# Optimization experiments

Measured on AMD Instinct MI355X. Metric: run time of the kernel, lower is better.

The kernel has to match this reference:

```python
import jax, jax.numpy as jnp
import numpy as np

# Module constants (match init_kwargs)
M = 2049                      # NpointsMesh (odd)
TAU = 2.821e-5                # Gaussian spreading width ~ 12*(pi/M)^2
XLIMS = (0.0, 10.0)
L = abs(XLIMS[1] - XLIMS[0])
KGRID = jnp.asarray(np.linspace(-(M // 2), M // 2, M), dtype=jnp.float32)        # (M,)
XGRID = jnp.asarray(2.0 * np.pi * np.linspace(XLIMS[0], XLIMS[1], M + 1)[:-1] / L,
                    dtype=jnp.float32)                                           # (M,)
FOUR_PI = 4.0 * np.pi


def setup_inputs() -> dict:
    key = jax.random.key(0)
    kx, = jax.random.split(key, 1)
    x = jax.random.uniform(kx, (16, 1024), dtype=jnp.float32) * 10.0  # points in [xLims[0], xLims[1])
    ones = jnp.ones((1,), dtype=jnp.float32)  # tf.initializers.ones for all 4 weights
    return {"x": x, "shift0": ones, "amp0": ones, "shift1": ones, "amp1": ones}


def reference(x, shift0, amp0, shift1, amp1):
    # Gaussian spreading: (B, N, M)
    diff = x[..., None] * (2.0 * np.pi / L) - XGRID
    g = jnp.exp(-jnp.square(diff) / (4.0 * TAU))
    # Sum over points -> gridded density (B, M), then FFT + shift
    gsum = jnp.sum(g, axis=1).astype(jnp.complex64)
    fft_g = jnp.fft.fftshift(jnp.fft.fft(gsum, axis=-1), axes=-1) * (L / (2.0 * np.pi))
    # Deconvolution of the Gaussian kernel (real-valued)
    deconv = jnp.sqrt(np.pi / TAU) * jnp.exp(jnp.square(KGRID) * TAU)  # (M,)
    rfft = fft_g * deconv  # (B, M) complex
    # Fourier multipliers (real; imag parts are structurally zero in the original)
    m1 = -amp0 * FOUR_PI / (jnp.square(KGRID) + jnp.square(5.0 * shift0))            # (M,)
    m2 = amp1 * FOUR_PI * jnp.square(1.0 / (jnp.square(KGRID) + jnp.square(5.0 * shift1)))  # (M,)
    mult = jnp.stack([m1, m2], axis=0)  # (2, M)
    mult_fft = mult[None, :, :].astype(jnp.complex64) * rfft[:, None, :]  # (B, 2, M)
    mult_deconv = mult_fft * deconv  # second deconv application, as in the original
    # Inverse FFT back to the mesh, keep real part: (B, 2, M)
    irfft = jnp.real(jnp.fft.ifft(jnp.fft.ifftshift(mult_deconv, axes=-1), axis=-1))
    # Inverse interpolation back to the points: (B, N, 2, M) -> (B, N, 2)
    local = irfft[:, None, :, :] * g[:, :, None, :]
    fmm = jnp.sum(local, axis=-1) / M
    return fmm
```

## Files before the change

kernel.cpp:

```cpp
#include <hip/hip_runtime.h>
#include <math.h>

#define M_   2049
#define B_   16
#define N_   1024
#define TAU_ 2.821e-5
#define PI_  3.14159265358979323846
#define TWO_PI_ 6.283185307179586476925286766559

#define GS_CH    8
#define H_JSPLIT 16
#define CV_SPLIT 8
#define FMM_LPP  16

__global__ void spread_h_kernel(const float* __restrict__ x,
                                const float* __restrict__ s0, const float* __restrict__ a0,
                                const float* __restrict__ s1, const float* __restrict__ a1,
                                double* __restrict__ gsum, double* __restrict__ hhalf) {
    __shared__ double smem[M_ + 64];
    const int bx = blockIdx.x;

    if (bx < GS_CH * B_) {
        const int b  = bx / GS_CH;
        const int ch = bx % GS_CH;
        for (int i = threadIdx.x; i < M_; i += 256) smem[i] = 0.0;
        __syncthreads();
        const int pl  = threadIdx.x >> 1;
        const int sub = threadIdx.x & 1;
        const double du      = TWO_PI_ / (double)M_;
        const double inv4tau = 1.0 / (4.0 * TAU_);
        const double u = (double)x[b * N_ + ch * (N_ / GS_CH) + pl] * (TWO_PI_ / 10.0);
        const int mc = (int)(u / du + 0.5);
        const int start = mc - 33 + sub * 34;
        for (int i = 0; i < 34; ++i) {
            int m = start + i;
            if (m >= 0 && m < M_) {
                double d = u - du * (double)m;
                double t = d * d * inv4tau;
                if (t < 88.0) atomicAdd(&smem[m], (double)__expf(-(float)t));
            }
        }
        __syncthreads();
        for (int i = threadIdx.x; i < M_; i += 256) {
            double v = smem[i];
            if (v != 0.0) atomicAdd(&gsum[b * M_ + i], v);
        }
    } else {
        const int t  = bx - GS_CH * B_;
        const int dt = t % 5;
        const int jc = (t / 5) % H_JSPLIT;
        const int c  = t / (5 * H_JSPLIT);
        double* costab = smem;
        double* coeff  = smem + M_;
        const int jlo = 1 + jc * (1024 / H_JSPLIT);
        const double ang0 = TWO_PI_ / (double)M_;

        for (int i = threadIdx.x; i <= 1024; i += 256) {
            double v = cos(ang0 * (double)i);
            costab[i] = v;
            if (i > 0) costab[M_ - i] = v;
        }
        if (threadIdx.x < 1024 / H_JSPLIT) {
            int j = jlo + threadIdx.x;
            double k2   = (double)j * (double)j;
            double dec2 = (PI_ / TAU_) * exp(2.0 * TAU_ * k2);
            double mult;
            if (c == 0) {
                double s = 5.0 * (double)s0[0];
                mult = -(double)a0[0] * 4.0 * PI_ / (k2 + s * s);
            } else {
                double s = 5.0 * (double)s1[0];
                double den = k2 + s * s;
                mult = (double)a1[0] * 4.0 * PI_ / (den * den);
            }
            coeff[threadIdx.x] = 2.0 * (10.0 / TWO_PI_) * dec2 * mult / (double)M_;
        }
        __syncthreads();

        const int d = dt * 256 + threadIdx.x;
        if (d > 1024) return;

        double acc = 0.0;
        if (jc == 0) {
            double mult0;
            if (c == 0) {
                double s = 5.0 * (double)s0[0];
                mult0 = -(double)a0[0] * 4.0 * PI_ / (s * s);
            } else {
                double s = 5.0 * (double)s1[0];
                mult0 = (double)a1[0] * 4.0 * PI_ / ((s * s) * (s * s));
            }
            acc = (10.0 / TWO_PI_) * (PI_ / TAU_) * mult0 / (double)M_;
        }
        int r = (int)(((long long)jlo * (long long)d) % M_);
        #pragma unroll 4
        for (int jj = 0; jj < 1024 / H_JSPLIT; ++jj) {
            acc += coeff[jj] * costab[r];
            r += d; if (r >= M_) r -= M_;
        }
        atomicAdd(&hhalf[c * 1025 + d], acc);
    }
}

__global__ void conv_kernel(const double* __restrict__ gsum, const double* __restrict__ hhalf,
                            double* __restrict__ conv) {
    __shared__ double hwin0[512];
    __shared__ double hwin1[512];
    const int mt = blockIdx.x;
    const int s  = blockIdx.y;
    const int b  = blockIdx.z;
    const int m0  = mt * 256;
    const int p0  = (s * M_) / CV_SPLIT;
    const int p1  = ((s + 1) * M_) / CV_SPLIT;
    const int len = p1 - p0;
    const int base = m0 - (p0 + len - 1) + M_;
    const int win  = 255 + len;
    for (int i = threadIdx.x; i < win; i += 256) {
        int idx = base + i;
        while (idx >= M_) idx -= M_;
        int d = (idx > 1024) ? (M_ - idx) : idx;
        hwin0[i] = hhalf[d];
        hwin1[i] = hhalf[1025 + d];
    }
    __syncthreads();
    const int m = m0 + threadIdx.x;
    if (m >= M_) return;
    const double* gs = gsum + (size_t)b * M_ + p0;
    const int i0 = threadIdx.x + len - 1;
    double a00 = 0.0, a01 = 0.0, a02 = 0.0, a03 = 0.0;
    double a10 = 0.0, a11 = 0.0, a12 = 0.0, a13 = 0.0;
    int mp = 0;
    for (; mp + 7 < len; mp += 8) {
        double g0 = gs[mp+0], g1 = gs[mp+1], g2 = gs[mp+2], g3 = gs[mp+3];
        double g4 = gs[mp+4], g5 = gs[mp+5], g6 = gs[mp+6], g7 = gs[mp+7];
        const double* h0 = hwin0 + (i0 - mp - 7);
        const double* h1 = hwin1 + (i0 - mp - 7);
        a00 += g0 * h0[7];  a10 += g0 * h1[7];
        a01 += g1 * h0[6];  a11 += g1 * h1[6];
        a02 += g2 * h0[5];  a12 += g2 * h1[5];
        a03 += g3 * h0[4];  a13 += g3 * h1[4];
        a00 += g4 * h0[3];  a10 += g4 * h1[3];
        a01 += g5 * h0[2];  a11 += g5 * h1[2];
        a02 += g6 * h0[1];  a12 += g6 * h1[1];
        a03 += g7 * h0[0];  a13 += g7 * h1[0];
    }
    for (; mp < len; ++mp) {
        double g = gs[mp];
        a00 += g * hwin0[i0 - mp];
        a10 += g * hwin1[i0 - mp];
    }
    double* cv = conv + (size_t)b * 2 * M_ + m;
    atomicAdd(cv,      (a00 + a01) + (a02 + a03));
    atomicAdd(cv + M_, (a10 + a11) + (a12 + a13));
}

__global__ void fmm_kernel(const float* __restrict__ x, const double* __restrict__ conv,
                           float* __restrict__ out) {
    const int gid = blockIdx.x * 256 + threadIdx.x;
    const int pt  = gid / FMM_LPP;
    const int sub = gid % FMM_LPP;
    const int b   = pt >> 10;
    const double du      = TWO_PI_ / (double)M_;
    const double inv4tau = 1.0 / (4.0 * TAU_);
    const double u = (double)x[pt] * (TWO_PI_ / 10.0);
    int mc = (int)(u / du + 0.5);
    int lo = mc - 34; if (lo < 0) lo = 0;
    int hi = mc + 34; if (hi > M_ - 1) hi = M_ - 1;
    const double* c0 = conv + (size_t)(b * 2) * M_;
    const double* c1 = c0 + M_;
    double a0 = 0.0, a1 = 0.0;
    for (int m = lo + sub; m <= hi; m += FMM_LPP) {
        double d = u - du * (double)m;
        double g = (double)__expf(-(float)(d * d * inv4tau));
        a0 += g * c0[m];
        a1 += g * c1[m];
    }
    a0 += __shfl_xor(a0, 1); a1 += __shfl_xor(a1, 1);
    a0 += __shfl_xor(a0, 2); a1 += __shfl_xor(a1, 2);
    a0 += __shfl_xor(a0, 4); a1 += __shfl_xor(a1, 4);
    a0 += __shfl_xor(a0, 8); a1 += __shfl_xor(a1, 8);
    if (sub == 0) {
        out[pt * 2 + 0] = (float)(a0 / (double)M_);
        out[pt * 2 + 1] = (float)(a1 / (double)M_);
    }
}

extern "C" void kernel_launch(void* const* d_in, const int* in_sizes, int n_in,
                              void* d_out, int out_size, void* d_ws, size_t ws_size,
                              hipStream_t stream) {
    (void)in_sizes; (void)n_in; (void)out_size; (void)ws_size;
    const float* x  = (const float*)d_in[0];
    const float* s0 = (const float*)d_in[1];
    const float* a0 = (const float*)d_in[2];
    const float* s1 = (const float*)d_in[3];
    const float* a1 = (const float*)d_in[4];
    float* out = (float*)d_out;

    double* gsum  = (double*)d_ws;
    double* hhalf = gsum + B_ * M_;
    double* conv  = hhalf + 2 * 1025;

    hipMemsetAsync(d_ws, 0, (size_t)(B_ * M_ + 2 * 1025 + B_ * 2 * M_) * sizeof(double), stream);

    hipLaunchKernelGGL(spread_h_kernel, dim3(GS_CH * B_ + 5 * H_JSPLIT * 2), dim3(256), 0,
                       stream, x, s0, a0, s1, a1, gsum, hhalf);
    hipLaunchKernelGGL(conv_kernel, dim3(9, CV_SPLIT, B_), dim3(256), 0, stream,
                       gsum, hhalf, conv);
    hipLaunchKernelGGL(fmm_kernel, dim3(B_ * N_ * FMM_LPP / 256), dim3(256), 0, stream,
                       x, conv, out);
}
```

Measured before the change: 97.92 us.

## Register-block circular convolution over 4 outputs per thread; merge both kernel channels

The convolution kernel now gives each thread 4 consecutive outputs and slides a register window over shared-memory kernel values, so every gsum load feeds 8 FMAs. Blocks cover 1024 outputs across 2 tiles, the split count doubles, and the last output (index 2048) is handled by a block reduction. The h-coefficient blocks now compute both multiplier channels from one cosine lookup, which halves those blocks. This cuts shared-memory traffic per FMA, at the cost of fewer blocks per batch and an extra reduction with barriers.

Measured after the change: 116.9 us. +19.4%, slower.

```diff
diff --git a/kernel.cpp b/kernel.cpp
--- a/kernel.cpp
+++ b/kernel.cpp
@@ -10,14 +10,14 @@
 
 #define GS_CH    8
 #define H_JSPLIT 16
-#define CV_SPLIT 8
+#define CV_SPLIT 16
 #define FMM_LPP  16
 
 __global__ void spread_h_kernel(const float* __restrict__ x,
                                 const float* __restrict__ s0, const float* __restrict__ a0,
                                 const float* __restrict__ s1, const float* __restrict__ a1,
                                 double* __restrict__ gsum, double* __restrict__ hhalf) {
-    __shared__ double smem[M_ + 64];
+    __shared__ double smem[M_ + 128];
     const int bx = blockIdx.x;
 
     if (bx < GS_CH * B_) {
@@ -48,10 +48,10 @@
     } else {
         const int t  = bx - GS_CH * B_;
         const int dt = t % 5;
-        const int jc = (t / 5) % H_JSPLIT;
-        const int c  = t / (5 * H_JSPLIT);
+        const int jc = t / 5;
         double* costab = smem;
-        double* coeff  = smem + M_;
+        double* cf0    = smem + M_;
+        double* cf1    = smem + M_ + 64;
         const int jlo = 1 + jc * (1024 / H_JSPLIT);
         const double ang0 = TWO_PI_ / (double)M_;
 
@@ -64,94 +64,110 @@
             int j = jlo + threadIdx.x;
             double k2   = (double)j * (double)j;
             double dec2 = (PI_ / TAU_) * exp(2.0 * TAU_ * k2);
-            double mult;
-            if (c == 0) {
-                double s = 5.0 * (double)s0[0];
-                mult = -(double)a0[0] * 4.0 * PI_ / (k2 + s * s);
-            } else {
-                double s = 5.0 * (double)s1[0];
-                double den = k2 + s * s;
-                mult = (double)a1[0] * 4.0 * PI_ / (den * den);
-            }
-            coeff[threadIdx.x] = 2.0 * (10.0 / TWO_PI_) * dec2 * mult / (double)M_;
+            double base = 2.0 * (10.0 / TWO_PI_) * dec2 / (double)M_;
+            double sA = 5.0 * (double)s0[0];
+            cf0[threadIdx.x] = base * (-(double)a0[0] * 4.0 * PI_ / (k2 + sA * sA));
+            double sB = 5.0 * (double)s1[0];
+            double den = k2 + sB * sB;
+            cf1[threadIdx.x] = base * ((double)a1[0] * 4.0 * PI_ / (den * den));
         }
         __syncthreads();
 
         const int d = dt * 256 + threadIdx.x;
         if (d > 1024) return;
 
-        double acc = 0.0;
+        double acc0 = 0.0, acc1 = 0.0;
         if (jc == 0) {
-            double mult0;
-            if (c == 0) {
-                double s = 5.0 * (double)s0[0];
-                mult0 = -(double)a0[0] * 4.0 * PI_ / (s * s);
-            } else {
-                double s = 5.0 * (double)s1[0];
-                mult0 = (double)a1[0] * 4.0 * PI_ / ((s * s) * (s * s));
-            }
-            acc = (10.0 / TWO_PI_) * (PI_ / TAU_) * mult0 / (double)M_;
+            double w0base = (10.0 / TWO_PI_) * (PI_ / TAU_) / (double)M_;
+            double sA = 5.0 * (double)s0[0];
+            acc0 = w0base * (-(double)a0[0] * 4.0 * PI_ / (sA * sA));
+            double sB = 5.0 * (double)s1[0];
+            acc1 = w0base * ((double)a1[0] * 4.0 * PI_ / ((sB * sB) * (sB * sB)));
         }
         int r = (int)(((long long)jlo * (long long)d) % M_);
         #pragma unroll 4
         for (int jj = 0; jj < 1024 / H_JSPLIT; ++jj) {
-            acc += coeff[jj] * costab[r];
+            double cv_ = costab[r];
+            acc0 += cf0[jj] * cv_;
+            acc1 += cf1[jj] * cv_;
             r += d; if (r >= M_) r -= M_;
         }
-        atomicAdd(&hhalf[c * 1025 + d], acc);
+        atomicAdd(&hhalf[d], acc0);
+        atomicAdd(&hhalf[1025 + d], acc1);
     }
 }
 
 __global__ void conv_kernel(const double* __restrict__ gsum, const double* __restrict__ hhalf,
                             double* __restrict__ conv) {
-    __shared__ double hwin0[512];
-    __shared__ double hwin1[512];
+    __shared__ double w0s[1160];
+    __shared__ double w1s[1160];
+    __shared__ double red[512];
     const int mt = blockIdx.x;
     const int s  = blockIdx.y;
     const int b  = blockIdx.z;
-    const int m0  = mt * 256;
+    const int m0  = mt * 1024;
     const int p0  = (s * M_) / CV_SPLIT;
     const int p1  = ((s + 1) * M_) / CV_SPLIT;
     const int len = p1 - p0;
-    const int base = m0 - (p0 + len - 1) + M_;
-    const int win  = 255 + len;
-    for (int i = threadIdx.x; i < win; i += 256) {
+    const int wcount = 1024 + len;
+    int base = m0 - (p0 + len - 1);
+    while (base < 0) base += M_;
+    for (int i = threadIdx.x; i < wcount; i += 256) {
         int idx = base + i;
         while (idx >= M_) idx -= M_;
         int d = (idx > 1024) ? (M_ - idx) : idx;
-        hwin0[i] = hhalf[d];
-        hwin1[i] = hhalf[1025 + d];
+        w0s[i] = hhalf[d];
+        w1s[i] = hhalf[1025 + d];
     }
     __syncthreads();
-    const int m = m0 + threadIdx.x;
-    if (m >= M_) return;
+
     const double* gs = gsum + (size_t)b * M_ + p0;
-    const int i0 = threadIdx.x + len - 1;
+
+    int q = 4 * threadIdx.x + len - 1;
+    double c0w0 = w0s[q],     c0w1 = w0s[q + 1], c0w2 = w0s[q + 2], c0w3 = w0s[q + 3];
+    double c1w0 = w1s[q],     c1w1 = w1s[q + 1], c1w2 = w1s[q + 2], c1w3 = w1s[q + 3];
     double a00 = 0.0, a01 = 0.0, a02 = 0.0, a03 = 0.0;
     double a10 = 0.0, a11 = 0.0, a12 = 0.0, a13 = 0.0;
-    int mp = 0;
-    for (; mp + 7 < len; mp += 8) {
-        double g0 = gs[mp+0], g1 = gs[mp+1], g2 = gs[mp+2], g3 = gs[mp+3];
-        double g4 = gs[mp+4], g5 = gs[mp+5], g6 = gs[mp+6], g7 = gs[mp+7];
-        const double* h0 = hwin0 + (i0 - mp - 7);
-        const double* h1 = hwin1 + (i0 - mp - 7);
-        a00 += g0 * h0[7];  a10 += g0 * h1[7];
-        a01 += g1 * h0[6];  a11 += g1 * h1[6];
-        a02 += g2 * h0[5];  a12 += g2 * h1[5];
-        a03 += g3 * h0[4];  a13 += g3 * h1[4];
-        a00 += g4 * h0[3];  a10 += g4 * h1[3];
-        a01 += g5 * h0[2];  a11 += g5 * h1[2];
-        a02 += g6 * h0[1];  a12 += g6 * h1[1];
-        a03 += g7 * h0[0];  a13 += g7 * h1[0];
-    }
-    for (; mp < len; ++mp) {
-        double g = gs[mp];
-        a00 += g * hwin0[i0 - mp];
-        a10 += g * hwin1[i0 - mp];
-    }
-    double* cv = conv + (size_t)b * 2 * M_ + m;
-    atomicAdd(cv,      (a00 + a01) + (a02 + a03));
-    atomicAdd(cv + M_, (a10 + a11) + (a12 + a13));
+    #pragma unroll 4
+    for (int t = 0; t < len; ++t) {
+        double g = gs[t];
+        a00 += g * c0w0; a01 += g * c0w1; a02 += g * c0w2; a03 += g * c0w3;
+        a10 += g * c1w0; a11 += g * c1w1; a12 += g * c1w2; a13 += g * c1w3;
+        c0w3 = c0w2; c0w2 = c0w1; c0w1 = c0w0;
+        c1w3 = c1w2; c1w2 = c1w1; c1w1 = c1w0;
+        --q;
+        c0w0 = w0s[q]; c1w0 = w1s[q];
+    }
+    {
+        double* cv = conv + (size_t)(b * 2) * M_ + m0 + 4 * threadIdx.x;
+        atomicAdd(cv + 0,      a00); atomicAdd(cv + 1,      a01);
+        atomicAdd(cv + 2,      a02); atomicAdd(cv + 3,      a03);
+        atomicAdd(cv + M_ + 0, a10); atomicAdd(cv + M_ + 1, a11);
+        atomicAdd(cv + M_ + 2, a12); atomicAdd(cv + M_ + 3, a13);
+    }
+
+    double t0 = 0.0, t1 = 0.0;
+    if (mt == 1 && threadIdx.x < len) {
+        double g = gs[threadIdx.x];
+        int qq = 1023 + len - threadIdx.x;
+        t0 = g * w0s[qq];
+        t1 = g * w1s[qq];
+    }
+    red[threadIdx.x]       = t0;
+    red[256 + threadIdx.x] = t1;
+    __syncthreads();
+    for (int off = 128; off > 0; off >>= 1) {
+        if (threadIdx.x < off) {
+            red[threadIdx.x]       += red[threadIdx.x + off];
+            red[256 + threadIdx.x] += red[256 + threadIdx.x + off];
+        }
+        __syncthreads();
+    }
+    if (mt == 1 && threadIdx.x == 0) {
+        double* cv = conv + (size_t)(b * 2) * M_;
+        atomicAdd(cv + 2048,      red[0]);
+        atomicAdd(cv + M_ + 2048, red[256]);
+    }
 }
 
 __global__ void fmm_kernel(const float* __restrict__ x, const double* __restrict__ conv,
@@ -202,9 +218,9 @@
 
     hipMemsetAsync(d_ws, 0, (size_t)(B_ * M_ + 2 * 1025 + B_ * 2 * M_) * sizeof(double), stream);
 
-    hipLaunchKernelGGL(spread_h_kernel, dim3(GS_CH * B_ + 5 * H_JSPLIT * 2), dim3(256), 0,
+    hipLaunchKernelGGL(spread_h_kernel, dim3(GS_CH * B_ + 5 * H_JSPLIT), dim3(256), 0,
                        stream, x, s0, a0, s1, a1, gsum, hhalf);
-    hipLaunchKernelGGL(conv_kernel, dim3(9, CV_SPLIT, B_), dim3(256), 0, stream,
+    hipLaunchKernelGGL(conv_kernel, dim3(2, CV_SPLIT, B_), dim3(256), 0, stream,
                        gsum, hhalf, conv);
     hipLaunchKernelGGL(fmm_kernel, dim3(B_ * N_ * FMM_LPP / 256), dim3(256), 0, stream,
                        x, conv, out);
```
